# Kernel tuning notes

Hardware: AMD Instinct MI355X
Metric: run time of the kernel (lower is better)

The kernel has to match this reference:

```python
import jax, jax.numpy as jnp
import numpy as np

N = 50000      # nodes
E = 800000     # edges (before self loops)
H = 8          # heads in first n_layer-1 GATConv layers
C = 16         # per-head channels (hidden/heads)
HID = 128      # hidden_channels
IN = 128       # in_dim
OUT = 10       # out_dim
G = 64         # number of graphs in batch
EPS = 1e-5     # BatchNorm eps
SLOPE = 0.2    # GATConv leaky_relu negative slope


def _gat_conv(x, src, dst, W, att_src, att_dst, bias, heads, ch):
    # x: [N, HID]; W: [HID, heads*ch]; att_*: [heads, ch]; bias: [heads*ch]
    h = (x @ W).reshape(N, heads, ch)                       # [N, h, c]
    a_src = jnp.sum(h * att_src, axis=-1)                   # [N, h]
    a_dst = jnp.sum(h * att_dst, axis=-1)                   # [N, h]
    e = jax.nn.leaky_relu(a_src[src] + a_dst[dst], SLOPE)   # [E', h]
    # numerically stable segment softmax over incoming edges of each dst node
    e = e - jax.ops.segment_max(e, dst, num_segments=N)[dst]
    ee = jnp.exp(e)
    denom = jax.ops.segment_sum(ee, dst, num_segments=N)[dst]
    alpha = ee / denom                                      # [E', h]
    out = jax.ops.segment_sum(h[src] * alpha[..., None], dst, num_segments=N)
    return out.reshape(N, heads * ch) + bias                # [N, heads*ch]


def _bn(x, gamma, beta):
    # PyG BatchNorm in training mode: batch stats over node dim (biased var)
    m = jnp.mean(x, axis=0)
    v = jnp.var(x, axis=0)
    return (x - m) * jax.lax.rsqrt(v + EPS) * gamma + beta


def setup_inputs() -> dict:
    key = jax.random.key(0)
    ks = jax.random.split(key, 24)
    s = 0.05
    inp = {
        "x": jax.random.normal(ks[0], (N, IN), jnp.float32),
        "edge_index": jax.random.randint(ks[1], (2, E), 0, N, jnp.int64),
        "cycle_index": jax.random.randint(ks[2], (2, 1000), 0, N, jnp.int64),
        "batch": jnp.sort(jax.random.randint(ks[3], (N,), 0, G, jnp.int64)),
        "W_emb": jax.random.normal(ks[4], (IN, HID), jnp.float32) * s,
        "b_emb": jnp.zeros((HID,), jnp.float32),
        "conv_W": jax.random.normal(ks[5], (2, HID, H * C), jnp.float32) * s,
        "conv_att_src": jax.random.normal(ks[6], (2, H, C), jnp.float32) * s,
        "conv_att_dst": jax.random.normal(ks[7], (2, H, C), jnp.float32) * s,
        "conv_b": jnp.zeros((2, H * C), jnp.float32),
        "conv2_W": jax.random.normal(ks[8], (HID, HID), jnp.float32) * s,
        "conv2_att_src": jax.random.normal(ks[9], (1, HID), jnp.float32) * s,
        "conv2_att_dst": jax.random.normal(ks[10], (1, HID), jnp.float32) * s,
        "conv2_b": jnp.zeros((HID,), jnp.float32),
        "bn_gamma": jnp.ones((3, HID), jnp.float32),
        "bn_beta": jnp.zeros((3, HID), jnp.float32),
        "lin1_W": jax.random.normal(ks[11], (HID, HID), jnp.float32) * s,
        "lin1_b": jnp.zeros((HID,), jnp.float32),
        "lin2_W": jax.random.normal(ks[12], (HID, HID), jnp.float32) * s,
        "lin2_b": jnp.zeros((HID,), jnp.float32),
        "lin3_W": jax.random.normal(ks[13], (HID, OUT), jnp.float32) * s,
        "lin3_b": jnp.zeros((OUT,), jnp.float32),
    }
    return inp


def reference(x, edge_index, cycle_index, batch, W_emb, b_emb, conv_W,
              conv_att_src, conv_att_dst, conv_b, conv2_W, conv2_att_src,
              conv2_att_dst, conv2_b, bn_gamma, bn_beta, lin1_W, lin1_b,
              lin2_W, lin2_b, lin3_W, lin3_b):
    # GATConv default add_self_loops=True
    loops = jnp.arange(N, dtype=edge_index.dtype)
    src = jnp.concatenate([edge_index[0], loops])
    dst = jnp.concatenate([edge_index[1], loops])

    h = x @ W_emb + b_emb  # dropout(p=0) is identity
    for i in range(3):
        if i < 2:
            c = _gat_conv(h, src, dst, conv_W[i], conv_att_src[i],
                          conv_att_dst[i], conv_b[i], H, C)
        else:
            c = _gat_conv(h, src, dst, conv2_W, conv2_att_src,
                          conv2_att_dst, conv2_b, 1, HID)
        h = jax.nn.relu(_bn(c, bn_gamma[i], bn_beta[i])) + h

    # global mean pool over graphs
    sums = jax.ops.segment_sum(h, batch, num_segments=G)
    cnts = jax.ops.segment_sum(jnp.ones((N, 1), h.dtype), batch, num_segments=G)
    pooled = sums / jnp.maximum(cnts, 1.0)

    out = jax.nn.relu(pooled @ lin1_W + lin1_b)
    out = jax.nn.relu(out @ lin2_W + lin2_b)
    return out @ lin3_W + lin3_b
```

## Files before the change

kernel.cpp:

```cpp
#include <hip/hip_runtime.h>


#define NN   50000
#define NE   800000
#define NET  (NE + NN)
#define HD   128
#define NG   64
#define NB   196
#define NBN  391
#define NCH  20
#define NTILE 3321
#define PSZ  6250

typedef unsigned short u16;
typedef __attribute__((ext_vector_type(8))) short short8;
typedef __attribute__((ext_vector_type(4))) float f32x4;

#define O_WEMB 0
#define O_BEMB 16384
#define O_CW   16512
#define O_CAS  49280
#define O_CAD  49536
#define O_CB   49792
#define O_C2W  50048
#define O_C2AS 66432
#define O_C2AD 66560
#define O_C2B  66688
#define O_BNG  66816
#define O_BNB  67200
#define O_L1W  67584
#define O_L1B  83968
#define O_L2W  84096
#define O_L2B  100480
#define O_L3W  100608
#define O_L3B  101888
#define NPAR   101898

__device__ int   g_f32flag;
__device__ __align__(16) u16 g_x [NN*HD];
__device__ __align__(16) u16 g_par[NPAR];
__device__ int   g_src[NE], g_dst[NE], g_batch[NN];
__device__ __align__(16) float g_h[NN*HD];
__device__ __align__(16) u16 g_hb[NN*HD];
__device__ __align__(16) u16 g_hw[NN*HD];
__device__ __align__(16) float g_c[NN*HD];
__device__ float g_asrc[NN*8];
__device__ float g_adst[NN*8];
__device__ int   g_rowptr[NN+1];
__device__ int   g_cursor[NN];
__device__ int   g_bsum[NB], g_boff[NB];
__device__ int   g_csr[NET];
__device__ float g_bnp1[NBN*HD], g_bnp2[NBN*HD];
__device__ float g_scl[HD], g_shf[HD];
__device__ int   g_gcnt[NG], g_goff[NG];
__device__ __align__(16) float g_poolp[NG*NCH*HD];
__device__ __align__(16) u16 g_WT[4][HD*HD];

__device__ __forceinline__ float b2f(u16 u) {
    unsigned v = ((unsigned)u) << 16; float f; __builtin_memcpy(&f, &v, 4); return f;
}
__device__ __forceinline__ u16 f2b(float f) {
    unsigned v; __builtin_memcpy(&v, &f, 4);
    return (u16)((v + 0x7fffu + ((v >> 16) & 1u)) >> 16);
}

__device__ __forceinline__ int probe_f32(const void* xp) {
    const u16* p = (const u16*)xp;
    int ex = (p[threadIdx.x & 63] >> 7) & 0xff;
    return __ballot(ex >= 0x93) != 0ULL;
}
__device__ __forceinline__ int probe_i64(const void* eip) {
    const int* q = (const int*)eip;
    return __ballot(q[2*(threadIdx.x & 63) + 1] != 0) == 0ULL;
}

__device__ __forceinline__ int block_incl_scan(int v, int* lds4) {
    int t = threadIdx.x, lane = t & 63, w = t >> 6;
    #pragma unroll
    for (int d = 1; d < 64; d <<= 1) {
        int o = __shfl_up(v, d);
        if (lane >= d) v += o;
    }
    if (lane == 63) lds4[w] = v;
    __syncthreads();
    if (w == 0 && lane < 4) {
        int s = lds4[lane];
        #pragma unroll
        for (int d = 1; d < 4; d <<= 1) {
            int o = __shfl_up(s, d);
            if (lane >= d) s += o;
        }
        lds4[lane] = s;
    }
    __syncthreads();
    if (w > 0) v += lds4[w-1];
    return v;
}

__global__ void k_convx(const void* xp) {
    int gi = blockIdx.x*256 + threadIdx.x;
    int f32 = probe_f32(xp);
    if (gi == 0) g_f32flag = f32;
    if (gi < NN) g_cursor[gi] = 1;
    int i = gi*4;
    if (f32) {
        float4 v = *(const float4*)((const float*)xp + i);
        ushort4 o = { f2b(v.x), f2b(v.y), f2b(v.z), f2b(v.w) };
        *(ushort4*)&g_x[i] = o;
    } else {
        *(ushort4*)&g_x[i] = *(const ushort4*)((const u16*)xp + i);
    }
}
struct P18 { const void* p[18]; int off[18]; int n[18]; };
__global__ void k_convpar(P18 a, const void* xp) {
    int f32 = probe_f32(xp);
    for (int t = 0; t < 18; ++t) {
        const void* s = a.p[t]; int off = a.off[t], n = a.n[t];
        for (int i = blockIdx.x*256 + threadIdx.x; i < n; i += 64*256)
            g_par[off+i] = f32 ? f2b(((const float*)s)[i]) : ((const u16*)s)[i];
    }
}
__global__ void k_convidx(const void* ei, const void* ba) {
    int i64 = probe_i64(ei);
    int e = blockIdx.x*256 + threadIdx.x;
    if (e < NE) {
        int s, d;
        if (i64) { s = (int)((const long long*)ei)[e]; d = (int)((const long long*)ei)[NE + e]; }
        else     { s = ((const int*)ei)[e];            d = ((const int*)ei)[NE + e]; }
        g_src[e] = s; g_dst[e] = d;
        atomicAdd(&g_cursor[d], 1);
    }
    if (e < NN)
        g_batch[e] = i64 ? (int)((const long long*)ba)[e] : ((const int*)ba)[e];
}

__global__ void k_blocksum() {
    int i = blockIdx.x*256 + threadIdx.x;
    int v = (i < NN) ? g_cursor[i] : 0;
    #pragma unroll
    for (int d = 32; d; d >>= 1) v += __shfl_down(v, d);
    __shared__ int lds[4];
    if ((threadIdx.x & 63) == 0) lds[threadIdx.x >> 6] = v;
    __syncthreads();
    if (threadIdx.x == 0) g_bsum[blockIdx.x] = lds[0]+lds[1]+lds[2]+lds[3];
}
__global__ void k_misc() {
    int b = blockIdx.x;
    if (b < 256) {
        int which = b >> 6;
        int poff = which==0 ? O_WEMB : which==1 ? O_CW : which==2 ? (O_CW+16384) : O_C2W;
        int idx = (b & 63)*256 + threadIdx.x;
        int n = idx >> 7, k = idx & 127;
        g_WT[which][n*HD + k] = g_par[poff + k*HD + n];
    } else if (b == 256) {
        __shared__ int lds[4];
        int t = threadIdx.x;
        int v = (t < NB) ? g_bsum[t] : 0;
        int incl = block_incl_scan(v, lds);
        if (t < NB) g_boff[t] = incl - v;
    } else {
        __shared__ int off[NG+1];
        int g = threadIdx.x;
        if (g <= NG) {
            int lo = 0, hi = NN;
            while (lo < hi) { int mid = (lo+hi) >> 1; if (g_batch[mid] < g) lo = mid+1; else hi = mid; }
            off[g] = lo;
        }
        __syncthreads();
        if (g < NG) { g_goff[g] = off[g]; g_gcnt[g] = off[g+1] - off[g]; }
    }
}
__global__ void k_downsweep() {
    __shared__ int lds[4];
    int i = blockIdx.x*256 + threadIdx.x;
    int c = (i < NN) ? g_cursor[i] : 0;
    int incl = block_incl_scan(c, lds);
    int base = g_boff[blockIdx.x];
    if (i < NN) {
        g_rowptr[i+1] = base + incl;
        g_cursor[i]   = base + incl - c;
    }
    if (i == 0) g_rowptr[0] = 0;
}

__global__ void k_scatter() {
    int part = blockIdx.x & 7;
    int e = (blockIdx.x >> 3)*256 + threadIdx.x;
    if (e >= NET) return;
    int s, d;
    if (e < NE) { s = g_src[e]; d = g_dst[e]; } else { s = d = e - NE; }
    if (d / PSZ != part) return;
    int pos = atomicAdd(&g_cursor[d], 1);
    g_csr[pos] = s;
}

__global__ __launch_bounds__(256) void k_gemm(int asel, int wsel, int biasoff,
                                              int outmode, int nrows,
                                              int asoff, int adoff, int heads) {
    __shared__ __align__(16) u16 wt[HD*136];
    const u16* A = asel ? g_hb : g_x;
    const u16* WTg = g_WT[wsel];
    int t = threadIdx.x;
    #pragma unroll
    for (int i = 0; i < 8; ++i) {
        int e = (t + i*256) * 8;
        int n = e >> 7, k = e & 127;
        *(uint4*)&wt[n*136 + k] = *(const uint4*)&WTg[e];
    }
    __syncthreads();
    int lane = t & 63, wave = t >> 6;
    int m16 = lane & 15, q = lane >> 4;
    int row0 = blockIdx.x*128 + wave*32;
    f32x4 acc[2][8];
    #pragma unroll
    for (int a = 0; a < 2; ++a)
        #pragma unroll
        for (int b = 0; b < 8; ++b) acc[a][b] = (f32x4){0.f,0.f,0.f,0.f};
    #pragma unroll
    for (int kc = 0; kc < 4; ++kc) {
        short8 af[2];
        #pragma unroll
        for (int rt = 0; rt < 2; ++rt) {
            int r = row0 + rt*16 + m16; if (r > nrows-1) r = nrows-1;
            af[rt] = *(const short8*)&A[r*HD + kc*32 + q*8];
        }
        #pragma unroll
        for (int ct = 0; ct < 8; ++ct) {
            short8 bf = *(const short8*)&wt[(ct*16 + m16)*136 + kc*32 + q*8];
            acc[0][ct] = __builtin_amdgcn_mfma_f32_16x16x32_bf16(af[0], bf, acc[0][ct], 0,0,0);
            acc[1][ct] = __builtin_amdgcn_mfma_f32_16x16x32_bf16(af[1], bf, acc[1][ct], 0,0,0);
        }
    }
    #pragma unroll
    for (int rt = 0; rt < 2; ++rt)
        #pragma unroll
        for (int reg = 0; reg < 4; ++reg) {
            int r = row0 + rt*16 + q*4 + reg;
            if (r < nrows) {
                #pragma unroll
                for (int ct = 0; ct < 8; ++ct) {
                    int c = ct*16 + m16;
                    float v = acc[rt][ct][reg];
                    if (biasoff >= 0) v += b2f(g_par[biasoff + c]);
                    if (outmode == 0) { g_h[r*HD+c] = v; g_hb[r*HD+c] = f2b(v); }
                    else              { g_hw[r*HD+c] = f2b(v); }
                }
            }
        }
    if (asoff >= 0) {
        #pragma unroll
        for (int rt = 0; rt < 2; ++rt)
            #pragma unroll
            for (int reg = 0; reg < 4; ++reg) {
                float v[8], u[8];
                #pragma unroll
                for (int ct = 0; ct < 8; ++ct) {
                    float w = acc[rt][ct][reg];
                    v[ct] = w * b2f(g_par[asoff + ct*16 + m16]);
                    u[ct] = w * b2f(g_par[adoff + ct*16 + m16]);
                }
                #pragma unroll
                for (int d = 1; d < 16; d <<= 1)
                    #pragma unroll
                    for (int ct = 0; ct < 8; ++ct) {
                        v[ct] += __shfl_xor(v[ct], d);
                        u[ct] += __shfl_xor(u[ct], d);
                    }
                int r = row0 + rt*16 + q*4 + reg;
                if (m16 == 0 && r < nrows) {
                    if (heads == 8) {
                        #pragma unroll
                        for (int h = 0; h < 8; ++h) {
                            g_asrc[r*8 + h] = v[h];
                            g_adst[r*8 + h] = u[h];
                        }
                    } else {
                        float sv = 0.f, su = 0.f;
                        #pragma unroll
                        for (int ct = 0; ct < 8; ++ct) { sv += v[ct]; su += u[ct]; }
                        g_asrc[r] = sv; g_adst[r] = su;
                    }
                }
            }
    }
}

__global__ __launch_bounds__(256) void k_flash(int boff, int heads, int hs) {
    int node = blockIdx.x*4 + (threadIdx.x >> 6);
    int lane = threadIdx.x & 63;
    int c0 = lane*2;
    int head = c0 >> hs;
    float ad = g_adst[node*heads + head];
    int beg = g_rowptr[node], end = g_rowptr[node+1];
    float l = 0.f, o0 = 0.f, o1 = 0.f;
    int j = beg;
    for (; j + 8 <= end; j += 8) {
        int s[8]; float av[8]; unsigned w[8];
        #pragma unroll
        for (int k = 0; k < 8; ++k) s[k] = g_csr[j+k];
        #pragma unroll
        for (int k = 0; k < 8; ++k) av[k] = g_asrc[s[k]*heads + head];
        #pragma unroll
        for (int k = 0; k < 8; ++k) w[k] = *(const unsigned*)&g_hw[s[k]*HD + c0];
        #pragma unroll
        for (int k = 0; k < 8; ++k) {
            float e = av[k] + ad;
            e = fmaxf(e, 0.2f*e);
            float p = __expf(fminf(e, 30.f));
            l  += p;
            o0 += p*b2f((u16)(w[k] & 0xffff));
            o1 += p*b2f((u16)(w[k] >> 16));
        }
    }
    for (; j + 4 <= end; j += 4) {
        int s[4]; float av[4]; unsigned w[4];
        #pragma unroll
        for (int k = 0; k < 4; ++k) s[k] = g_csr[j+k];
        #pragma unroll
        for (int k = 0; k < 4; ++k) av[k] = g_asrc[s[k]*heads + head];
        #pragma unroll
        for (int k = 0; k < 4; ++k) w[k] = *(const unsigned*)&g_hw[s[k]*HD + c0];
        #pragma unroll
        for (int k = 0; k < 4; ++k) {
            float e = av[k] + ad;
            e = fmaxf(e, 0.2f*e);
            float p = __expf(fminf(e, 30.f));
            l  += p;
            o0 += p*b2f((u16)(w[k] & 0xffff));
            o1 += p*b2f((u16)(w[k] >> 16));
        }
    }
    for (; j < end; ++j) {
        int s = g_csr[j];
        float e = g_asrc[s*heads + head] + ad;
        e = fmaxf(e, 0.2f*e);
        float p = __expf(fminf(e, 30.f));
        unsigned w = *(const unsigned*)&g_hw[s*HD + c0];
        l  += p;
        o0 += p*b2f((u16)(w & 0xffff));
        o1 += p*b2f((u16)(w >> 16));
    }
    float inv = 1.f/l;
    g_c[node*HD + c0]     = o0*inv + b2f(g_par[boff + c0]);
    g_c[node*HD + c0 + 1] = o1*inv + b2f(g_par[boff + c0 + 1]);
}

__global__ void k_bnstats() {
    int t = threadIdx.x; int ch = t & 127, r0 = t >> 7;
    int base = blockIdx.x*128;
    float s = 0.f, q = 0.f;
    for (int i = r0; i < 128; i += 2) {
        int n = base + i;
        if (n < NN) { float v = g_c[n*HD + ch]; s += v; q += v*v; }
    }
    __shared__ float sS[256], sQ[256];
    sS[t] = s; sQ[t] = q; __syncthreads();
    if (t < 128) {
        g_bnp1[blockIdx.x*HD + t] = sS[t] + sS[t+128];
        g_bnp2[blockIdx.x*HD + t] = sQ[t] + sQ[t+128];
    }
}
__global__ void k_bnfinal(int goff, int boff) {
    int ch = blockIdx.x, t = threadIdx.x;
    float s = 0.f, q = 0.f;
    for (int b = t; b < NBN; b += 64) { s += g_bnp1[b*HD + ch]; q += g_bnp2[b*HD + ch]; }
    #pragma unroll
    for (int d = 32; d; d >>= 1) { s += __shfl_down(s, d); q += __shfl_down(q, d); }
    if (t == 0) {
        float mean = s / (float)NN;
        float var  = fmaxf(q / (float)NN - mean*mean, 0.f);
        float sc = b2f(g_par[goff + ch]) * rsqrtf(var + 1e-5f);
        g_scl[ch] = sc;
        g_shf[ch] = b2f(g_par[boff + ch]) - mean*sc;
    }
}
__global__ void k_bnapply(int writeb) {
    int i = (blockIdx.x*256 + threadIdx.x)*4;
    int ch = i & 127;
    float4 c = *(const float4*)&g_c[i];
    float4 h = *(const float4*)&g_h[i];
    float4 r;
    r.x = fmaxf(c.x*g_scl[ch  ] + g_shf[ch  ], 0.f) + h.x;
    r.y = fmaxf(c.y*g_scl[ch+1] + g_shf[ch+1], 0.f) + h.y;
    r.z = fmaxf(c.z*g_scl[ch+2] + g_shf[ch+2], 0.f) + h.z;
    r.w = fmaxf(c.w*g_scl[ch+3] + g_shf[ch+3], 0.f) + h.w;
    *(float4*)&g_h[i] = r;
    if (writeb) {
        ushort4 o = { f2b(r.x), f2b(r.y), f2b(r.z), f2b(r.w) };
        *(ushort4*)&g_hb[i] = o;
    }
}

__global__ void k_pool() {
    int g = blockIdx.x / NCH, c = blockIdx.x - g*NCH;
    int cnt = g_gcnt[g], off = g_goff[g];
    int step = (cnt + NCH - 1) / NCH;
    int r0 = c*step, r1 = min(cnt, r0 + step);
    int t = threadIdx.x;
    int ch = (t & 31) * 4;
    int rr = t >> 5;
    float4 s = {0.f,0.f,0.f,0.f};
    for (int i = r0 + rr; i < r1; i += 8) {
        float4 v = *(const float4*)&g_h[(off + i)*HD + ch];
        s.x += v.x; s.y += v.y; s.z += v.z; s.w += v.w;
    }
    __shared__ float4 sh[256];
    sh[t] = s; __syncthreads();
    if (t < 32) {
        float4 a = sh[t];
        #pragma unroll
        for (int k = 1; k < 8; ++k) {
            float4 b = sh[t + k*32];
            a.x += b.x; a.y += b.y; a.z += b.z; a.w += b.w;
        }
        *(float4*)&g_poolp[(g*NCH + c)*HD + ch] = a;
    }
}

__global__ void k_head(void* outB) {
    __shared__ float pl[HD], h1[HD], h2[HD];
    int g = blockIdx.x, t = threadIdx.x;
    float s = 0.f;
    for (int c = 0; c < NCH; ++c) s += g_poolp[(g*NCH + c)*HD + t];
    pl[t] = s / fmaxf((float)g_gcnt[g], 1.f);
    __syncthreads();
    float acc = b2f(g_par[O_L1B + t]);
    for (int k = 0; k < HD; ++k) acc += pl[k] * b2f(g_par[O_L1W + k*HD + t]);
    h1[t] = fmaxf(acc, 0.f);
    __syncthreads();
    acc = b2f(g_par[O_L2B + t]);
    for (int k = 0; k < HD; ++k) acc += h1[k] * b2f(g_par[O_L2W + k*HD + t]);
    h2[t] = fmaxf(acc, 0.f);
    __syncthreads();
    if (t < 10) {
        acc = b2f(g_par[O_L3B + t]);
        for (int k = 0; k < HD; ++k) acc += h2[k] * b2f(g_par[O_L3W + k*10 + t]);
        if (g_f32flag) ((float*)outB)[g*10 + t] = acc;
        else           ((u16*)outB)[g*10 + t] = f2b(acc);
    }
}

extern "C" void kernel_launch(void* const* d_in, const int* in_sizes, int n_in,
                              void* d_out, int out_size, void* d_ws, size_t ws_size,
                              hipStream_t stream) {
    const void* x     = d_in[0];
    const void* ei    = d_in[1];
    const void* batch = d_in[3];

    k_convx<<<6250, 256, 0, stream>>>(x);
    P18 a;
    const int srcidx[18] = {4,5,6,7,8,9,10,11,12,13,14,15,16,17,18,19,20,21};
    const int offs[18] = {O_WEMB,O_BEMB,O_CW,O_CAS,O_CAD,O_CB,O_C2W,O_C2AS,O_C2AD,
                          O_C2B,O_BNG,O_BNB,O_L1W,O_L1B,O_L2W,O_L2B,O_L3W,O_L3B};
    const int lens[18] = {16384,128,32768,256,256,256,16384,128,128,128,384,384,
                          16384,128,16384,128,1280,10};
    for (int t = 0; t < 18; ++t) { a.p[t] = d_in[srcidx[t]]; a.off[t] = offs[t]; a.n[t] = lens[t]; }
    k_convpar<<<64, 256, 0, stream>>>(a, x);
    k_convidx<<<3125, 256, 0, stream>>>(ei, batch);

    k_blocksum<<<NB, 256, 0, stream>>>();
    k_misc<<<258, 256, 0, stream>>>();
    k_downsweep<<<NB, 256, 0, stream>>>();
    k_scatter<<<NTILE*8, 256, 0, stream>>>();

    k_gemm<<<391, 256, 0, stream>>>(0, 0, O_BEMB, 0, NN, -1, -1, 0);

    for (int L = 0; L < 3; ++L) {
        int heads = (L < 2) ? 8 : 1;
        int hs    = (L < 2) ? 4 : 7;
        int as    = (L < 2) ? O_CAS + L*128 : O_C2AS;
        int ad    = (L < 2) ? O_CAD + L*128 : O_C2AD;
        int cb    = (L < 2) ? O_CB  + L*128 : O_C2B;
        k_gemm<<<391, 256, 0, stream>>>(1, L+1, -1, 1, NN, as, ad, heads);
        k_flash<<<12500, 256, 0, stream>>>(cb, heads, hs);
        k_bnstats<<<NBN, 256, 0, stream>>>();
        k_bnfinal<<<128, 64, 0, stream>>>(O_BNG + L*HD, O_BNB + L*HD);
        k_bnapply<<<6250, 256, 0, stream>>>(L < 2 ? 1 : 0);
    }

    k_pool<<<NG*NCH, 256, 0, stream>>>();
    k_head<<<NG, 128, 0, stream>>>(d_out);
}
```

Baseline: 574.4 us.

## Fuse BatchNorm apply into next GEMM A-load and pooling; store conv output in bf16

Removes the separate BatchNorm-apply kernel. The next layer's GEMM now computes relu(bn(c)) + h on the fly while loading its A fragments, writes the updated fp32 residual back, and uses the bf16 value as MFMA input. The final layer's apply moves into the pooling reduction. The conv output buffer g_c changes from fp32 to bf16 to halve its read and write traffic, which lowers BN-stat precision slightly. Clamped tail rows in the last GEMM block can read and rewrite the same g_h row from several threads, a possible race on the final node.

New measurement: 552.9 us. -3.8%, faster.

```diff
diff --git a/kernel.cpp b/kernel.cpp
--- a/kernel.cpp
+++ b/kernel.cpp
@@ -43,7 +43,7 @@
 __device__ __align__(16) float g_h[NN*HD];
 __device__ __align__(16) u16 g_hb[NN*HD];
 __device__ __align__(16) u16 g_hw[NN*HD];
-__device__ __align__(16) float g_c[NN*HD];
+__device__ __align__(16) u16 g_c[NN*HD];
 __device__ float g_asrc[NN*8];
 __device__ float g_adst[NN*8];
 __device__ int   g_rowptr[NN+1];
@@ -196,8 +196,10 @@
 
 __global__ __launch_bounds__(256) void k_gemm(int asel, int wsel, int biasoff,
                                               int outmode, int nrows,
-                                              int asoff, int adoff, int heads) {
+                                              int asoff, int adoff, int heads,
+                                              int bnfuse) {
     __shared__ __align__(16) u16 wt[HD*136];
+    __shared__ float s_scl[HD], s_shf[HD];
     const u16* A = asel ? g_hb : g_x;
     const u16* WTg = g_WT[wsel];
     int t = threadIdx.x;
@@ -207,6 +209,7 @@
         int n = e >> 7, k = e & 127;
         *(uint4*)&wt[n*136 + k] = *(const uint4*)&WTg[e];
     }
+    if (bnfuse && t < HD) { s_scl[t] = g_scl[t]; s_shf[t] = g_shf[t]; }
     __syncthreads();
     int lane = t & 63, wave = t >> 6;
     int m16 = lane & 15, q = lane >> 4;
@@ -222,7 +225,27 @@
         #pragma unroll
         for (int rt = 0; rt < 2; ++rt) {
             int r = row0 + rt*16 + m16; if (r > nrows-1) r = nrows-1;
-            af[rt] = *(const short8*)&A[r*HD + kc*32 + q*8];
+            int base = r*HD + kc*32 + q*8;
+            if (bnfuse) {
+                short8 cv = *(const short8*)&g_c[base];
+                float4 h0 = *(const float4*)&g_h[base];
+                float4 h1 = *(const float4*)&g_h[base+4];
+                float nh[8];
+                #pragma unroll
+                for (int k2 = 0; k2 < 8; ++k2) {
+                    int ch = kc*32 + q*8 + k2;
+                    float hv = (k2 < 4) ? (&h0.x)[k2] : (&h1.x)[k2-4];
+                    float v = fmaxf(b2f((u16)cv[k2])*s_scl[ch] + s_shf[ch], 0.f) + hv;
+                    nh[k2] = v;
+                    af[rt][k2] = (short)f2b(v);
+                }
+                float4 o0 = {nh[0],nh[1],nh[2],nh[3]};
+                float4 o1 = {nh[4],nh[5],nh[6],nh[7]};
+                *(float4*)&g_h[base]   = o0;
+                *(float4*)&g_h[base+4] = o1;
+            } else {
+                af[rt] = *(const short8*)&A[base];
+            }
         }
         #pragma unroll
         for (int ct = 0; ct < 8; ++ct) {
@@ -341,8 +364,9 @@
         o1 += p*b2f((u16)(w >> 16));
     }
     float inv = 1.f/l;
-    g_c[node*HD + c0]     = o0*inv + b2f(g_par[boff + c0]);
-    g_c[node*HD + c0 + 1] = o1*inv + b2f(g_par[boff + c0 + 1]);
+    ushort2 o = { f2b(o0*inv + b2f(g_par[boff + c0])),
+                  f2b(o1*inv + b2f(g_par[boff + c0 + 1])) };
+    *(ushort2*)&g_c[node*HD + c0] = o;
 }
 
 __global__ void k_bnstats() {
@@ -351,7 +375,7 @@
     float s = 0.f, q = 0.f;
     for (int i = r0; i < 128; i += 2) {
         int n = base + i;
-        if (n < NN) { float v = g_c[n*HD + ch]; s += v; q += v*v; }
+        if (n < NN) { float v = b2f(g_c[n*HD + ch]); s += v; q += v*v; }
     }
     __shared__ float sS[256], sQ[256];
     sS[t] = s; sQ[t] = q; __syncthreads();
@@ -372,22 +396,6 @@
         float sc = b2f(g_par[goff + ch]) * rsqrtf(var + 1e-5f);
         g_scl[ch] = sc;
         g_shf[ch] = b2f(g_par[boff + ch]) - mean*sc;
-    }
-}
-__global__ void k_bnapply(int writeb) {
-    int i = (blockIdx.x*256 + threadIdx.x)*4;
-    int ch = i & 127;
-    float4 c = *(const float4*)&g_c[i];
-    float4 h = *(const float4*)&g_h[i];
-    float4 r;
-    r.x = fmaxf(c.x*g_scl[ch  ] + g_shf[ch  ], 0.f) + h.x;
-    r.y = fmaxf(c.y*g_scl[ch+1] + g_shf[ch+1], 0.f) + h.y;
-    r.z = fmaxf(c.z*g_scl[ch+2] + g_shf[ch+2], 0.f) + h.z;
-    r.w = fmaxf(c.w*g_scl[ch+3] + g_shf[ch+3], 0.f) + h.w;
-    *(float4*)&g_h[i] = r;
-    if (writeb) {
-        ushort4 o = { f2b(r.x), f2b(r.y), f2b(r.z), f2b(r.w) };
-        *(ushort4*)&g_hb[i] = o;
     }
 }
 
@@ -399,10 +407,17 @@
     int t = threadIdx.x;
     int ch = (t & 31) * 4;
     int rr = t >> 5;
+    float sc0 = g_scl[ch], sc1 = g_scl[ch+1], sc2 = g_scl[ch+2], sc3 = g_scl[ch+3];
+    float sf0 = g_shf[ch], sf1 = g_shf[ch+1], sf2 = g_shf[ch+2], sf3 = g_shf[ch+3];
     float4 s = {0.f,0.f,0.f,0.f};
     for (int i = r0 + rr; i < r1; i += 8) {
-        float4 v = *(const float4*)&g_h[(off + i)*HD + ch];
-        s.x += v.x; s.y += v.y; s.z += v.z; s.w += v.w;
+        int base = (off + i)*HD + ch;
+        ushort4 cv = *(const ushort4*)&g_c[base];
+        float4 hv = *(const float4*)&g_h[base];
+        s.x += fmaxf(b2f(cv.x)*sc0 + sf0, 0.f) + hv.x;
+        s.y += fmaxf(b2f(cv.y)*sc1 + sf1, 0.f) + hv.y;
+        s.z += fmaxf(b2f(cv.z)*sc2 + sf2, 0.f) + hv.z;
+        s.w += fmaxf(b2f(cv.w)*sc3 + sf3, 0.f) + hv.w;
     }
     __shared__ float4 sh[256];
     sh[t] = s; __syncthreads();
@@ -463,7 +478,7 @@
     k_downsweep<<<NB, 256, 0, stream>>>();
     k_scatter<<<NTILE*8, 256, 0, stream>>>();
 
-    k_gemm<<<391, 256, 0, stream>>>(0, 0, O_BEMB, 0, NN, -1, -1, 0);
+    k_gemm<<<391, 256, 0, stream>>>(0, 0, O_BEMB, 0, NN, -1, -1, 0, 0);
 
     for (int L = 0; L < 3; ++L) {
         int heads = (L < 2) ? 8 : 1;
@@ -471,11 +486,10 @@
         int as    = (L < 2) ? O_CAS + L*128 : O_C2AS;
         int ad    = (L < 2) ? O_CAD + L*128 : O_C2AD;
         int cb    = (L < 2) ? O_CB  + L*128 : O_C2B;
-        k_gemm<<<391, 256, 0, stream>>>(1, L+1, -1, 1, NN, as, ad, heads);
+        k_gemm<<<391, 256, 0, stream>>>(1, L+1, -1, 1, NN, as, ad, heads, L > 0 ? 1 : 0);
         k_flash<<<12500, 256, 0, stream>>>(cb, heads, hs);
         k_bnstats<<<NBN, 256, 0, stream>>>();
         k_bnfinal<<<128, 64, 0, stream>>>(O_BNG + L*HD, O_BNB + L*HD);
-        k_bnapply<<<6250, 256, 0, stream>>>(L < 2 ? 1 : 0);
     }
 
     k_pool<<<NG*NCH, 256, 0, stream>>>();
```
